# Kernel tuning notes

Measured on AMD Instinct MI355X. Metric: run time of the kernel, lower is better.

Reference implementation:

```python
import jax, jax.numpy as jnp
import numpy as np

SFREQ = 100
NPERSEG = 100  # min(n_times=200, 100)
NOVERLAP = NPERSEG // 2

# periodic hann window (scipy get_window('hann', N) with sym=False)
_WIN_NP = 0.5 - 0.5 * np.cos(2.0 * np.pi * np.arange(NPERSEG) / NPERSEG)
_WIN_SQ_SUM = float(np.sum(_WIN_NP ** 2))
_FREQS = np.fft.rfftfreq(NPERSEG, 1.0 / SFREQ)  # 0..50 Hz, 51 bins
_BANDS = [(0.5, 4.0), (4.0, 8.0), (8.0, 13.0), (13.0, 30.0)]  # delta/theta/alpha/beta
_BAND_IDX = [np.where((_FREQS >= lo) & (_FREQS <= hi))[0] for lo, hi in _BANDS]


def welch_band_features(x):
    """Batched Welch PSD band powers. x: (B,C,T) -> (B, C*4)."""
    B, C, T = x.shape
    step = NPERSEG - NOVERLAP
    n_seg = (T - NPERSEG) // step + 1
    seg_idx = np.arange(n_seg)[:, None] * step + np.arange(NPERSEG)  # (S, L)
    segs = x[..., seg_idx]                              # (B,C,S,L)
    segs = segs - segs.mean(-1, keepdims=True)          # detrend='constant'
    win = jnp.asarray(_WIN_NP, x.dtype)
    spec = jnp.fft.rfft(segs * win, axis=-1)            # (B,C,S,F)
    scale = 1.0 / (SFREQ * _WIN_SQ_SUM)
    psd = (spec.real ** 2 + spec.imag ** 2) * scale
    psd = psd.at[..., 1:-1].multiply(2.0)               # one-sided, nfft even
    psd = psd.mean(-2)                                  # average over segments -> (B,C,F)
    feats = jnp.stack([psd[..., idx].mean(-1) for idx in _BAND_IDX], axis=-1)  # (B,C,4)
    return feats.reshape(B, C * 4)


def setup_inputs() -> dict:
    key = jax.random.key(0)
    ks = jax.random.split(key, 16)
    B, C, T = 2048, 129, 200
    red = C // 8  # 16
    s = 0.05
    inp = {
        "x": jax.random.normal(ks[0], (B, C, T), jnp.float32),
        # channel attention fc (no bias)
        "w_att1": jax.random.normal(ks[1], (C, red), jnp.float32) * s,
        "w_att2": jax.random.normal(ks[2], (red, C), jnp.float32) * s,
        # stand-in EEGNeX backbone: time-mean pool + linear C->64
        "w_bb": jax.random.normal(ks[3], (C, 64), jnp.float32) * s,
        "b_bb": jnp.zeros((64,), jnp.float32),
        # freq encoder
        "w_fe1": jax.random.normal(ks[4], (C * 4, 128), jnp.float32) * s,
        "b_fe1": jnp.zeros((128,), jnp.float32),
        "w_fe2": jax.random.normal(ks[5], (128, 64), jnp.float32) * s,
        "b_fe2": jnp.zeros((64,), jnp.float32),
        # head
        "w_h1": jax.random.normal(ks[6], (128, 128), jnp.float32) * s,
        "b_h1": jnp.zeros((128,), jnp.float32),
        "w_h2": jax.random.normal(ks[7], (128, 64), jnp.float32) * s,
        "b_h2": jnp.zeros((64,), jnp.float32),
        "w_h3": jax.random.normal(ks[8], (64, 1), jnp.float32) * s,
        "b_h3": jnp.zeros((1,), jnp.float32),
    }
    return inp


def reference(x, w_att1, w_att2, w_bb, b_bb, w_fe1, b_fe1, w_fe2, b_fe2,
              w_h1, b_h1, w_h2, b_h2, w_h3, b_h3):
    # --- channel attention ---
    avg = x.mean(-1)                                    # (B,C)
    mx = x.max(-1)                                      # (B,C)
    fc = lambda v: jax.nn.relu(v @ w_att1) @ w_att2
    att = jax.nn.sigmoid(fc(avg) + fc(mx))[..., None]   # (B,C,1)
    x_att = x * att
    # --- backbone (stand-in for EEGNeXBase): time pool + linear ---
    time_feat = jax.nn.relu(x_att.mean(-1) @ w_bb + b_bb)  # (B,64)
    # --- frequency branch (computed from raw x, detached in original) ---
    freq = welch_band_features(jax.lax.stop_gradient(x))   # (B, C*4)
    freq = jax.nn.relu(freq @ w_fe1 + b_fe1)
    freq = jax.nn.relu(freq @ w_fe2 + b_fe2)               # (B,64)
    # --- head ---
    h = jnp.concatenate([time_feat, freq], axis=1)         # (B,128)
    h = jax.nn.relu(h @ w_h1 + b_h1)
    h = jax.nn.relu(h @ w_h2 + b_h2)
    return h @ w_h3 + b_h3                                  # (B,1)
```

## Files before the change

kernel.cpp:

```cpp
#include <hip/hip_runtime.h>
#include <math.h>

constexpr int BB = 2048;
constexpr int CC = 129;
constexpr int TT = 200;
constexpr int NPAIR = BB * CC;
constexpr int PPB = 64;
constexpr int XSTR = 201;

constexpr int OFF_AVG = 8192;
constexpr int OFF_MX  = OFF_AVG + NPAIR;
constexpr int OFF_FT  = OFF_MX + NPAIR;

__global__ void kInit(float2* __restrict__ tab) {
    int i = blockIdx.x * 256 + threadIdx.x;
    if (i >= 3000) return;
    int r = i / 100, t = i % 100;
    int ph = ((r + 1) * t) % 100;
    const float C = 0.06283185307179587f;
    float w = 0.5f - 0.5f * cosf(C * (float)t);
    float ang = C * (float)ph;
    tab[i] = make_float2(w * cosf(ang), w * sinf(ang));
}

template<int KB, int NB, bool STATS>
__device__ __forceinline__ void do_wave(const float* __restrict__ xp,
                                        const float* __restrict__ tbf,
                                        float* __restrict__ bs,
                                        int pair,
                                        float* __restrict__ avg,
                                        float* __restrict__ mxg) {
    const float* trow = tbf + (KB - 1) * 200;
    float re[NB][3], im[NB][3];
    #pragma unroll
    for (int b = 0; b < NB; b++)
        #pragma unroll
        for (int s = 0; s < 3; s++) { re[b][s] = 0.f; im[b][s] = 0.f; }
    float h0 = 0.f, h1 = 0.f, h2 = 0.f, h3 = 0.f, m = -3.4e38f;

    auto run = [&](int t0, int t1, float& hA, float& hC) {
        for (int t = t0; t < t1; t += 2) {
            float a0 = xp[t],       a1 = xp[t + 1];
            float b0 = xp[t + 50],  b1 = xp[t + 51];
            float c0 = xp[t + 100], c1 = xp[t + 101];
            if (STATS) {
                hA += a0 + a1; hC += c0 + c1;
                m = fmaxf(m, fmaxf(fmaxf(a0, a1), fmaxf(c0, c1)));
            }
            #pragma unroll
            for (int b = 0; b < NB; b++) {
                float4 w = *(const float4*)(trow + b * 200 + 2 * t);
                re[b][0] += a0 * w.x; im[b][0] += a0 * w.y;
                re[b][0] += a1 * w.z; im[b][0] += a1 * w.w;
                re[b][1] += b0 * w.x; im[b][1] += b0 * w.y;
                re[b][1] += b1 * w.z; im[b][1] += b1 * w.w;
                re[b][2] += c0 * w.x; im[b][2] += c0 * w.y;
                re[b][2] += c1 * w.z; im[b][2] += c1 * w.w;
            }
        }
    };
    run(0, 50, h0, h2);
    run(50, 100, h1, h3);

    if (STATS) {
        float mu0 = (h0 + h1) * 0.01f, mu1 = (h1 + h2) * 0.01f, mu2 = (h2 + h3) * 0.01f;
        re[0][0] += 25.f * mu0;
        re[0][1] += 25.f * mu1;
        re[0][2] += 25.f * mu2;
        avg[pair] = (h0 + h1 + h2 + h3) * (1.f / 200.f);
        mxg[pair] = m;
    }

    float s0 = 0.f, s1 = 0.f, s2 = 0.f, s3 = 0.f;
    #pragma unroll
    for (int b = 0; b < NB; b++) {
        int k = KB + b;
        float v = re[b][0] * re[b][0] + im[b][0] * im[b][0]
                + re[b][1] * re[b][1] + im[b][1] * im[b][1]
                + re[b][2] * re[b][2] + im[b][2] * im[b][2];
        if (k >= 1  && k <= 4)  s0 += v;
        if (k >= 4  && k <= 8)  s1 += v;
        if (k >= 8  && k <= 13) s2 += v;
        if (k >= 13 && k <= 30) s3 += v;
    }
    if (KB <= 4)                       atomicAdd(&bs[0], s0);
    if (KB <= 8 && KB + NB - 1 >= 4)   atomicAdd(&bs[1], s1);
    if (KB <= 13 && KB + NB - 1 >= 8)  atomicAdd(&bs[2], s2);
    if (KB + NB - 1 >= 13)             atomicAdd(&bs[3], s3);
}

__global__ __launch_bounds__(256, 2) void kA(const float* __restrict__ x,
                                             const float2* __restrict__ tabg,
                                             float* __restrict__ avg,
                                             float* __restrict__ mxg,
                                             float* __restrict__ feat) {
    __shared__ __align__(16) float xs[PPB * XSTR];
    __shared__ __align__(16) float tbf[6000];
    __shared__ float bsum[PPB][4];

    const int tid = threadIdx.x;
    const int blk = blockIdx.x;

    {
        const float4* tg = (const float4*)tabg;
        float4* td = (float4*)tbf;
        for (int i = tid; i < 1500; i += 256) td[i] = tg[i];
    }
    {
        const float4* xg = (const float4*)(x + (size_t)blk * PPB * TT);
        for (int i = tid; i < 3200; i += 256) {
            float4 v = xg[i];
            int p = i / 50, t4 = (i % 50) * 4;
            float* d = &xs[p * XSTR + t4];
            d[0] = v.x; d[1] = v.y; d[2] = v.z; d[3] = v.w;
        }
    }
    ((float*)bsum)[tid] = 0.f;
    __syncthreads();

    const int wv = tid >> 6, p = tid & 63;
    const float* xp = &xs[p * XSTR];
    float* bs = &bsum[p][0];
    const int pair = blk * PPB + p;

    if      (wv == 0) do_wave<1,  6, true >(xp, tbf, bs, pair, avg, mxg);
    else if (wv == 1) do_wave<7,  8, false>(xp, tbf, bs, pair, avg, mxg);
    else if (wv == 2) do_wave<15, 8, false>(xp, tbf, bs, pair, avg, mxg);
    else              do_wave<23, 8, false>(xp, tbf, bs, pair, avg, mxg);

    __syncthreads();
    {
        int pp = tid >> 2, bb = tid & 3;
        const float cnt[4] = {4.f, 5.f, 6.f, 18.f};
        feat[(size_t)(blk * PPB + pp) * 4 + bb] = bsum[pp][bb] * (2.f / (11250.f * cnt[bb]));
    }
}

__global__ __launch_bounds__(256) void kB(const float* __restrict__ avg,
                                          const float* __restrict__ mxv,
                                          const float* __restrict__ feat,
                                          const float* __restrict__ w_att1,
                                          const float* __restrict__ w_att2,
                                          const float* __restrict__ w_bb,
                                          const float* __restrict__ b_bb,
                                          const float* __restrict__ w_fe1,
                                          const float* __restrict__ b_fe1,
                                          const float* __restrict__ w_fe2,
                                          const float* __restrict__ b_fe2,
                                          const float* __restrict__ w_h1,
                                          const float* __restrict__ b_h1,
                                          const float* __restrict__ w_h2,
                                          const float* __restrict__ b_h2,
                                          const float* __restrict__ w_h3,
                                          const float* __restrict__ b_h3,
                                          float* __restrict__ out) {
    __shared__ __align__(16) float s_avg[258], s_mx[258], s_fq[1032];
    __shared__ float s_t1[32];
    __shared__ __align__(16) float s_v[258], s_h[256], s_f1[256], s_g1[256], s_g2[128];

    const int b = blockIdx.x;
    const int tid = threadIdx.x;

    for (int i = tid; i < 258; i += 256) { s_avg[i] = avg[b * 258 + i]; s_mx[i] = mxv[b * 258 + i]; }
    for (int i = tid; i < 1032; i += 256) s_fq[i] = feat[(size_t)b * 1032 + i];
    __syncthreads();

    if (tid < 32) {
        int r = tid >> 4, h = tid & 15;
        const float* pa = &s_avg[r * 129];
        const float* pm = &s_mx[r * 129];
        float a = 0.f, m = 0.f;
        for (int c = 0; c < 129; c++) {
            float w = w_att1[c * 16 + h];
            a += pa[c] * w; m += pm[c] * w;
        }
        s_t1[r * 16 + h] = fmaxf(a, 0.f) + fmaxf(m, 0.f);
    }
    __syncthreads();

    for (int i = tid; i < 258; i += 256) {
        int r = i / 129, c = i - r * 129;
        const float* t1 = &s_t1[r * 16];
        float l = 0.f;
        #pragma unroll
        for (int j = 0; j < 16; j++) l += t1[j] * w_att2[j * 129 + c];
        s_v[i] = s_avg[i] / (1.f + expf(-l));
    }
    __syncthreads();

    if (tid < 128) {
        int r = tid >> 6, o = tid & 63;
        const float* v = &s_v[r * 129];
        float acc = b_bb[o];
        for (int c = 0; c < 129; c++) acc += v[c] * w_bb[c * 64 + o];
        s_h[r * 128 + o] = fmaxf(acc, 0.f);
    }
    {
        int r = tid >> 7, o = tid & 127;
        const float* fq = &s_fq[r * 516];
        float acc = b_fe1[o];
        for (int i = 0; i < 516; i += 4) {
            float4 q = *(const float4*)(fq + i);
            acc += q.x * w_fe1[(i    ) * 128 + o];
            acc += q.y * w_fe1[(i + 1) * 128 + o];
            acc += q.z * w_fe1[(i + 2) * 128 + o];
            acc += q.w * w_fe1[(i + 3) * 128 + o];
        }
        s_f1[r * 128 + o] = fmaxf(acc, 0.f);
    }
    __syncthreads();

    if (tid < 128) {
        int r = tid >> 6, o = tid & 63;
        const float* f = &s_f1[r * 128];
        float acc = b_fe2[o];
        for (int i = 0; i < 128; i += 4) {
            float4 q = *(const float4*)(f + i);
            acc += q.x * w_fe2[(i    ) * 64 + o];
            acc += q.y * w_fe2[(i + 1) * 64 + o];
            acc += q.z * w_fe2[(i + 2) * 64 + o];
            acc += q.w * w_fe2[(i + 3) * 64 + o];
        }
        s_h[r * 128 + 64 + o] = fmaxf(acc, 0.f);
    }
    __syncthreads();

    {
        int r = tid >> 7, o = tid & 127;
        const float* hh = &s_h[r * 128];
        float acc = b_h1[o];
        for (int i = 0; i < 128; i += 4) {
            float4 q = *(const float4*)(hh + i);
            acc += q.x * w_h1[(i    ) * 128 + o];
            acc += q.y * w_h1[(i + 1) * 128 + o];
            acc += q.z * w_h1[(i + 2) * 128 + o];
            acc += q.w * w_h1[(i + 3) * 128 + o];
        }
        s_g1[r * 128 + o] = fmaxf(acc, 0.f);
    }
    __syncthreads();

    if (tid < 128) {
        int r = tid >> 6, o = tid & 63;
        const float* g = &s_g1[r * 128];
        float acc = b_h2[o];
        for (int i = 0; i < 128; i += 4) {
            float4 q = *(const float4*)(g + i);
            acc += q.x * w_h2[(i    ) * 64 + o];
            acc += q.y * w_h2[(i + 1) * 64 + o];
            acc += q.z * w_h2[(i + 2) * 64 + o];
            acc += q.w * w_h2[(i + 3) * 64 + o];
        }
        s_g2[r * 64 + o] = fmaxf(acc, 0.f);
    }
    __syncthreads();

    if (tid < 128) {
        int r = tid >> 6, o = tid & 63;
        float pz = s_g2[r * 64 + o] * w_h3[o];
        for (int off = 32; off >= 1; off >>= 1) pz += __shfl_xor(pz, off, 64);
        if (o == 0) out[b * 2 + r] = pz + b_h3[0];
    }
}

extern "C" void kernel_launch(void* const* d_in, const int* in_sizes, int n_in,
                              void* d_out, int out_size, void* d_ws, size_t ws_size,
                              hipStream_t stream) {
    const float* x      = (const float*)d_in[0];
    const float* w_att1 = (const float*)d_in[1];
    const float* w_att2 = (const float*)d_in[2];
    const float* w_bb   = (const float*)d_in[3];
    const float* b_bb   = (const float*)d_in[4];
    const float* w_fe1  = (const float*)d_in[5];
    const float* b_fe1  = (const float*)d_in[6];
    const float* w_fe2  = (const float*)d_in[7];
    const float* b_fe2  = (const float*)d_in[8];
    const float* w_h1   = (const float*)d_in[9];
    const float* b_h1   = (const float*)d_in[10];
    const float* w_h2   = (const float*)d_in[11];
    const float* b_h2   = (const float*)d_in[12];
    const float* w_h3   = (const float*)d_in[13];
    const float* b_h3   = (const float*)d_in[14];

    float* ws = (float*)d_ws;
    float2* tab = (float2*)ws;
    float* avg = ws + OFF_AVG;
    float* mxv = ws + OFF_MX;
    float* feat = ws + OFF_FT;

    kInit<<<12, 256, 0, stream>>>(tab);
    kA<<<NPAIR / PPB, 256, 0, stream>>>(x, (const float2*)tab, avg, mxv, feat);
    kB<<<BB / 2, 256, 0, stream>>>(avg, mxv, feat,
                                   w_att1, w_att2, w_bb, b_bb,
                                   w_fe1, b_fe1, w_fe2, b_fe2,
                                   w_h1, b_h1, w_h2, b_h2, w_h3, b_h3,
                                   (float*)d_out);
}
```

Baseline: 494.0 us.

## Split DFT bins across 8 waves, vectorize LDS reads, and split-K the MLP kernel

The Welch kernel now runs 512 threads per block, so eight waves each cover four frequency bins instead of four waves covering six to eight. The mean/max statistics move into a separate vectorized pass on wave 0. The x tile stride is padded to 204 so rows are 16-byte aligned, which allows float4 stores and loads in LDS, and the DFT inner loop is unrolled four samples at a time. The MLP kernel now handles one batch row per block, with split-K partial sums across all 256 threads for each layer. This adds more syncs and a redundant extra pass over x in LDS for the statistics, and the larger block may reduce per-thread register budget.

```diff
diff --git a/kernel.cpp b/kernel.cpp
--- a/kernel.cpp
+++ b/kernel.cpp
@@ -6,7 +6,7 @@
 constexpr int TT = 200;
 constexpr int NPAIR = BB * CC;
 constexpr int PPB = 64;
-constexpr int XSTR = 201;
+constexpr int XSTR = 204;
 
 constexpr int OFF_AVG = 8192;
 constexpr int OFF_MX  = OFF_AVG + NPAIR;
@@ -23,52 +23,46 @@
     tab[i] = make_float2(w * cosf(ang), w * sinf(ang));
 }
 
-template<int KB, int NB, bool STATS>
-__device__ __forceinline__ void do_wave(const float* __restrict__ xp,
-                                        const float* __restrict__ tbf,
-                                        float* __restrict__ bs,
-                                        int pair,
-                                        float* __restrict__ avg,
-                                        float* __restrict__ mxg) {
+template<int KB, int NB>
+__device__ __forceinline__ void dft_wave(const float* __restrict__ xp,
+                                         const float* __restrict__ tbf,
+                                         float* __restrict__ bs,
+                                         float mu0, float mu1, float mu2) {
     const float* trow = tbf + (KB - 1) * 200;
     float re[NB][3], im[NB][3];
     #pragma unroll
     for (int b = 0; b < NB; b++)
         #pragma unroll
         for (int s = 0; s < 3; s++) { re[b][s] = 0.f; im[b][s] = 0.f; }
-    float h0 = 0.f, h1 = 0.f, h2 = 0.f, h3 = 0.f, m = -3.4e38f;
-
-    auto run = [&](int t0, int t1, float& hA, float& hC) {
-        for (int t = t0; t < t1; t += 2) {
-            float a0 = xp[t],       a1 = xp[t + 1];
-            float b0 = xp[t + 50],  b1 = xp[t + 51];
-            float c0 = xp[t + 100], c1 = xp[t + 101];
-            if (STATS) {
-                hA += a0 + a1; hC += c0 + c1;
-                m = fmaxf(m, fmaxf(fmaxf(a0, a1), fmaxf(c0, c1)));
+
+    #pragma unroll 5
+    for (int t0 = 0; t0 < 100; t0 += 4) {
+        float4 a  = *(const float4*)(xp + t0);
+        float2 b0 = *(const float2*)(xp + t0 + 50);
+        float2 b1 = *(const float2*)(xp + t0 + 52);
+        float4 c  = *(const float4*)(xp + t0 + 100);
+        float xa[4] = {a.x, a.y, a.z, a.w};
+        float xb[4] = {b0.x, b0.y, b1.x, b1.y};
+        float xc[4] = {c.x, c.y, c.z, c.w};
+        #pragma unroll
+        for (int b = 0; b < NB; b++) {
+            float4 w0 = *(const float4*)(trow + b * 200 + 2 * t0);
+            float4 w1 = *(const float4*)(trow + b * 200 + 2 * t0 + 4);
+            float cs[4] = {w0.x, w0.z, w1.x, w1.z};
+            float sn[4] = {w0.y, w0.w, w1.y, w1.w};
+            #pragma unroll
+            for (int u = 0; u < 4; u++) {
+                re[b][0] += xa[u] * cs[u];  im[b][0] += xa[u] * sn[u];
+                re[b][1] += xb[u] * cs[u];  im[b][1] += xb[u] * sn[u];
+                re[b][2] += xc[u] * cs[u];  im[b][2] += xc[u] * sn[u];
             }
-            #pragma unroll
-            for (int b = 0; b < NB; b++) {
-                float4 w = *(const float4*)(trow + b * 200 + 2 * t);
-                re[b][0] += a0 * w.x; im[b][0] += a0 * w.y;
-                re[b][0] += a1 * w.z; im[b][0] += a1 * w.w;
-                re[b][1] += b0 * w.x; im[b][1] += b0 * w.y;
-                re[b][1] += b1 * w.z; im[b][1] += b1 * w.w;
-                re[b][2] += c0 * w.x; im[b][2] += c0 * w.y;
-                re[b][2] += c1 * w.z; im[b][2] += c1 * w.w;
-            }
-        }
-    };
-    run(0, 50, h0, h2);
-    run(50, 100, h1, h3);
-
-    if (STATS) {
-        float mu0 = (h0 + h1) * 0.01f, mu1 = (h1 + h2) * 0.01f, mu2 = (h2 + h3) * 0.01f;
+        }
+    }
+
+    if (KB == 1) {
         re[0][0] += 25.f * mu0;
         re[0][1] += 25.f * mu1;
         re[0][2] += 25.f * mu2;
-        avg[pair] = (h0 + h1 + h2 + h3) * (1.f / 200.f);
-        mxg[pair] = m;
     }
 
     float s0 = 0.f, s1 = 0.f, s2 = 0.f, s3 = 0.f;
@@ -81,7 +75,7 @@
         if (k >= 1  && k <= 4)  s0 += v;
         if (k >= 4  && k <= 8)  s1 += v;
         if (k >= 8  && k <= 13) s2 += v;
-        if (k >= 13 && k <= 30) s3 += v;
+        if (k >= 13)            s3 += v;
     }
     if (KB <= 4)                       atomicAdd(&bs[0], s0);
     if (KB <= 8 && KB + NB - 1 >= 4)   atomicAdd(&bs[1], s1);
@@ -89,7 +83,7 @@
     if (KB + NB - 1 >= 13)             atomicAdd(&bs[3], s3);
 }
 
-__global__ __launch_bounds__(256, 2) void kA(const float* __restrict__ x,
+__global__ __launch_bounds__(512, 4) void kA(const float* __restrict__ x,
                                              const float2* __restrict__ tabg,
                                              float* __restrict__ avg,
                                              float* __restrict__ mxg,
@@ -104,162 +98,194 @@
     {
         const float4* tg = (const float4*)tabg;
         float4* td = (float4*)tbf;
-        for (int i = tid; i < 1500; i += 256) td[i] = tg[i];
+        for (int i = tid; i < 1500; i += 512) td[i] = tg[i];
     }
     {
         const float4* xg = (const float4*)(x + (size_t)blk * PPB * TT);
-        for (int i = tid; i < 3200; i += 256) {
+        for (int i = tid; i < 3200; i += 512) {
             float4 v = xg[i];
             int p = i / 50, t4 = (i % 50) * 4;
-            float* d = &xs[p * XSTR + t4];
-            d[0] = v.x; d[1] = v.y; d[2] = v.z; d[3] = v.w;
-        }
-    }
-    ((float*)bsum)[tid] = 0.f;
+            *(float4*)(xs + p * XSTR + t4) = v;
+        }
+    }
+    if (tid < 256) ((float*)bsum)[tid] = 0.f;
     __syncthreads();
 
     const int wv = tid >> 6, p = tid & 63;
-    const float* xp = &xs[p * XSTR];
-    float* bs = &bsum[p][0];
-    const int pair = blk * PPB + p;
-
-    if      (wv == 0) do_wave<1,  6, true >(xp, tbf, bs, pair, avg, mxg);
-    else if (wv == 1) do_wave<7,  8, false>(xp, tbf, bs, pair, avg, mxg);
-    else if (wv == 2) do_wave<15, 8, false>(xp, tbf, bs, pair, avg, mxg);
-    else              do_wave<23, 8, false>(xp, tbf, bs, pair, avg, mxg);
-
-    __syncthreads();
-    {
+    const float* xp = xs + p * XSTR;
+    float* bs = bsum[p];
+
+    float mu0 = 0.f, mu1 = 0.f, mu2 = 0.f;
+    if (wv == 0) {
+        float h0 = 0.f, h1 = 0.f, h2 = 0.f, h3 = 0.f, m = -3.4e38f;
+        #pragma unroll
+        for (int i = 0; i < 12; i++) {
+            float4 v = *(const float4*)(xp + i * 4);
+            h0 += (v.x + v.y) + (v.z + v.w);
+            m = fmaxf(m, fmaxf(fmaxf(v.x, v.y), fmaxf(v.z, v.w)));
+        }
+        {   float4 v = *(const float4*)(xp + 48);
+            h0 += v.x + v.y; h1 += v.z + v.w;
+            m = fmaxf(m, fmaxf(fmaxf(v.x, v.y), fmaxf(v.z, v.w))); }
+        #pragma unroll
+        for (int i = 13; i < 25; i++) {
+            float4 v = *(const float4*)(xp + i * 4);
+            h1 += (v.x + v.y) + (v.z + v.w);
+            m = fmaxf(m, fmaxf(fmaxf(v.x, v.y), fmaxf(v.z, v.w)));
+        }
+        #pragma unroll
+        for (int i = 25; i < 37; i++) {
+            float4 v = *(const float4*)(xp + i * 4);
+            h2 += (v.x + v.y) + (v.z + v.w);
+            m = fmaxf(m, fmaxf(fmaxf(v.x, v.y), fmaxf(v.z, v.w)));
+        }
+        {   float4 v = *(const float4*)(xp + 148);
+            h2 += v.x + v.y; h3 += v.z + v.w;
+            m = fmaxf(m, fmaxf(fmaxf(v.x, v.y), fmaxf(v.z, v.w))); }
+        #pragma unroll
+        for (int i = 38; i < 50; i++) {
+            float4 v = *(const float4*)(xp + i * 4);
+            h3 += (v.x + v.y) + (v.z + v.w);
+            m = fmaxf(m, fmaxf(fmaxf(v.x, v.y), fmaxf(v.z, v.w)));
+        }
+        int pair = blk * PPB + p;
+        avg[pair] = (h0 + h1 + h2 + h3) * (1.f / 200.f);
+        mxg[pair] = m;
+        mu0 = (h0 + h1) * 0.01f; mu1 = (h1 + h2) * 0.01f; mu2 = (h2 + h3) * 0.01f;
+    }
+
+    switch (wv) {
+        case 0: dft_wave<1,  2>(xp, tbf, bs, mu0, mu1, mu2); break;
+        case 1: dft_wave<3,  4>(xp, tbf, bs, 0, 0, 0); break;
+        case 2: dft_wave<7,  4>(xp, tbf, bs, 0, 0, 0); break;
+        case 3: dft_wave<11, 4>(xp, tbf, bs, 0, 0, 0); break;
+        case 4: dft_wave<15, 4>(xp, tbf, bs, 0, 0, 0); break;
+        case 5: dft_wave<19, 4>(xp, tbf, bs, 0, 0, 0); break;
+        case 6: dft_wave<23, 4>(xp, tbf, bs, 0, 0, 0); break;
+        default: dft_wave<27, 4>(xp, tbf, bs, 0, 0, 0); break;
+    }
+
+    __syncthreads();
+    if (tid < 256) {
         int pp = tid >> 2, bb = tid & 3;
         const float cnt[4] = {4.f, 5.f, 6.f, 18.f};
         feat[(size_t)(blk * PPB + pp) * 4 + bb] = bsum[pp][bb] * (2.f / (11250.f * cnt[bb]));
     }
 }
 
-__global__ __launch_bounds__(256) void kB(const float* __restrict__ avg,
-                                          const float* __restrict__ mxv,
-                                          const float* __restrict__ feat,
-                                          const float* __restrict__ w_att1,
-                                          const float* __restrict__ w_att2,
-                                          const float* __restrict__ w_bb,
-                                          const float* __restrict__ b_bb,
-                                          const float* __restrict__ w_fe1,
-                                          const float* __restrict__ b_fe1,
-                                          const float* __restrict__ w_fe2,
-                                          const float* __restrict__ b_fe2,
-                                          const float* __restrict__ w_h1,
-                                          const float* __restrict__ b_h1,
-                                          const float* __restrict__ w_h2,
-                                          const float* __restrict__ b_h2,
-                                          const float* __restrict__ w_h3,
-                                          const float* __restrict__ b_h3,
-                                          float* __restrict__ out) {
-    __shared__ __align__(16) float s_avg[258], s_mx[258], s_fq[1032];
-    __shared__ float s_t1[32];
-    __shared__ __align__(16) float s_v[258], s_h[256], s_f1[256], s_g1[256], s_g2[128];
+__global__ __launch_bounds__(256, 8) void kB(const float* __restrict__ avg,
+                                             const float* __restrict__ mxv,
+                                             const float* __restrict__ feat,
+                                             const float* __restrict__ w_att1,
+                                             const float* __restrict__ w_att2,
+                                             const float* __restrict__ w_bb,
+                                             const float* __restrict__ b_bb,
+                                             const float* __restrict__ w_fe1,
+                                             const float* __restrict__ b_fe1,
+                                             const float* __restrict__ w_fe2,
+                                             const float* __restrict__ b_fe2,
+                                             const float* __restrict__ w_h1,
+                                             const float* __restrict__ b_h1,
+                                             const float* __restrict__ w_h2,
+                                             const float* __restrict__ b_h2,
+                                             const float* __restrict__ w_h3,
+                                             const float* __restrict__ b_h3,
+                                             float* __restrict__ out) {
+    __shared__ float s_avg[132], s_mx[132], s_fq[520];
+    __shared__ float s_t1a[16], s_t1b[16], s_t1[16];
+    __shared__ float s_v[132];
+    __shared__ float s_tf[2][64];
+    __shared__ float s_p1[2][128];
+    __shared__ float s_f1[128];
+    __shared__ float s_p2[4][64];
+    __shared__ float s_h[128];
+    __shared__ float s_pg1[2][128];
+    __shared__ float s_g1[128];
+    __shared__ float s_pg2[4][64];
 
     const int b = blockIdx.x;
     const int tid = threadIdx.x;
 
-    for (int i = tid; i < 258; i += 256) { s_avg[i] = avg[b * 258 + i]; s_mx[i] = mxv[b * 258 + i]; }
-    for (int i = tid; i < 1032; i += 256) s_fq[i] = feat[(size_t)b * 1032 + i];
+    for (int i = tid; i < 129; i += 256) { s_avg[i] = avg[b * 129 + i]; s_mx[i] = mxv[b * 129 + i]; }
+    for (int i = tid; i < 516; i += 256) s_fq[i] = feat[(size_t)b * 516 + i];
     __syncthreads();
 
     if (tid < 32) {
-        int r = tid >> 4, h = tid & 15;
-        const float* pa = &s_avg[r * 129];
-        const float* pm = &s_mx[r * 129];
-        float a = 0.f, m = 0.f;
-        for (int c = 0; c < 129; c++) {
-            float w = w_att1[c * 16 + h];
-            a += pa[c] * w; m += pm[c] * w;
-        }
-        s_t1[r * 16 + h] = fmaxf(a, 0.f) + fmaxf(m, 0.f);
-    }
-    __syncthreads();
-
-    for (int i = tid; i < 258; i += 256) {
-        int r = i / 129, c = i - r * 129;
-        const float* t1 = &s_t1[r * 16];
+        int h = tid & 15;
+        const float* src = (tid >= 16) ? s_mx : s_avg;
+        float acc = 0.f;
+        #pragma unroll 4
+        for (int c = 0; c < 129; c++) acc += src[c] * w_att1[c * 16 + h];
+        ((tid >= 16) ? s_t1b : s_t1a)[h] = fmaxf(acc, 0.f);
+    }
+    __syncthreads();
+    if (tid < 16) s_t1[tid] = s_t1a[tid] + s_t1b[tid];
+    __syncthreads();
+
+    if (tid < 129) {
         float l = 0.f;
         #pragma unroll
-        for (int j = 0; j < 16; j++) l += t1[j] * w_att2[j * 129 + c];
-        s_v[i] = s_avg[i] / (1.f + expf(-l));
+        for (int j = 0; j < 16; j++) l += s_t1[j] * w_att2[j * 129 + tid];
+        s_v[tid] = s_avg[tid] / (1.f + expf(-l));
     }
     __syncthreads();
 
     if (tid < 128) {
-        int r = tid >> 6, o = tid & 63;
-        const float* v = &s_v[r * 129];
-        float acc = b_bb[o];
-        for (int c = 0; c < 129; c++) acc += v[c] * w_bb[c * 64 + o];
-        s_h[r * 128 + o] = fmaxf(acc, 0.f);
-    }
-    {
-        int r = tid >> 7, o = tid & 127;
-        const float* fq = &s_fq[r * 516];
-        float acc = b_fe1[o];
-        for (int i = 0; i < 516; i += 4) {
-            float4 q = *(const float4*)(fq + i);
-            acc += q.x * w_fe1[(i    ) * 128 + o];
-            acc += q.y * w_fe1[(i + 1) * 128 + o];
-            acc += q.z * w_fe1[(i + 2) * 128 + o];
-            acc += q.w * w_fe1[(i + 3) * 128 + o];
-        }
-        s_f1[r * 128 + o] = fmaxf(acc, 0.f);
-    }
-    __syncthreads();
-
-    if (tid < 128) {
-        int r = tid >> 6, o = tid & 63;
-        const float* f = &s_f1[r * 128];
-        float acc = b_fe2[o];
-        for (int i = 0; i < 128; i += 4) {
-            float4 q = *(const float4*)(f + i);
-            acc += q.x * w_fe2[(i    ) * 64 + o];
-            acc += q.y * w_fe2[(i + 1) * 64 + o];
-            acc += q.z * w_fe2[(i + 2) * 64 + o];
-            acc += q.w * w_fe2[(i + 3) * 64 + o];
-        }
-        s_h[r * 128 + 64 + o] = fmaxf(acc, 0.f);
-    }
-    __syncthreads();
-
-    {
-        int r = tid >> 7, o = tid & 127;
-        const float* hh = &s_h[r * 128];
-        float acc = b_h1[o];
-        for (int i = 0; i < 128; i += 4) {
-            float4 q = *(const float4*)(hh + i);
-            acc += q.x * w_h1[(i    ) * 128 + o];
-            acc += q.y * w_h1[(i + 1) * 128 + o];
-            acc += q.z * w_h1[(i + 2) * 128 + o];
-            acc += q.w * w_h1[(i + 3) * 128 + o];
-        }
-        s_g1[r * 128 + o] = fmaxf(acc, 0.f);
-    }
-    __syncthreads();
-
-    if (tid < 128) {
-        int r = tid >> 6, o = tid & 63;
-        const float* g = &s_g1[r * 128];
-        float acc = b_h2[o];
-        for (int i = 0; i < 128; i += 4) {
-            float4 q = *(const float4*)(g + i);
-            acc += q.x * w_h2[(i    ) * 64 + o];
-            acc += q.y * w_h2[(i + 1) * 64 + o];
-            acc += q.z * w_h2[(i + 2) * 64 + o];
-            acc += q.w * w_h2[(i + 3) * 64 + o];
-        }
-        s_g2[r * 64 + o] = fmaxf(acc, 0.f);
-    }
-    __syncthreads();
-
-    if (tid < 128) {
-        int r = tid >> 6, o = tid & 63;
-        float pz = s_g2[r * 64 + o] * w_h3[o];
+        int o = tid & 63, ks = tid >> 6;
+        int i0 = ks ? 65 : 0, i1 = ks ? 129 : 65;
+        float acc = 0.f;
+        #pragma unroll 4
+        for (int i = i0; i < i1; i++) acc += s_v[i] * w_bb[i * 64 + o];
+        s_tf[ks][o] = acc;
+    }
+    {
+        int o = tid & 127, ks = tid >> 7;
+        float acc = 0.f;
+        #pragma unroll 4
+        for (int i = ks * 258; i < ks * 258 + 258; i++) acc += s_fq[i] * w_fe1[i * 128 + o];
+        s_p1[ks][o] = acc;
+    }
+    __syncthreads();
+    if (tid < 64) s_h[tid] = fmaxf(s_tf[0][tid] + s_tf[1][tid] + b_bb[tid], 0.f);
+    if (tid >= 128) { int o = tid - 128; s_f1[o] = fmaxf(s_p1[0][o] + s_p1[1][o] + b_fe1[o], 0.f); }
+    __syncthreads();
+
+    {
+        int o = tid & 63, ks = tid >> 6;
+        float acc = 0.f;
+        #pragma unroll 4
+        for (int i = ks * 32; i < ks * 32 + 32; i++) acc += s_f1[i] * w_fe2[i * 64 + o];
+        s_p2[ks][o] = acc;
+    }
+    __syncthreads();
+    if (tid < 64) s_h[64 + tid] = fmaxf(s_p2[0][tid] + s_p2[1][tid] + s_p2[2][tid] + s_p2[3][tid] + b_fe2[tid], 0.f);
+    __syncthreads();
+
+    {
+        int o = tid & 127, ks = tid >> 7;
+        float acc = 0.f;
+        #pragma unroll 4
+        for (int i = ks * 64; i < ks * 64 + 64; i++) acc += s_h[i] * w_h1[i * 128 + o];
+        s_pg1[ks][o] = acc;
+    }
+    __syncthreads();
+    if (tid < 128) s_g1[tid] = fmaxf(s_pg1[0][tid] + s_pg1[1][tid] + b_h1[tid], 0.f);
+    __syncthreads();
+
+    {
+        int o = tid & 63, ks = tid >> 6;
+        float acc = 0.f;
+        #pragma unroll 4
+        for (int i = ks * 32; i < ks * 32 + 32; i++) acc += s_g1[i] * w_h2[i * 64 + o];
+        s_pg2[ks][o] = acc;
+    }
+    __syncthreads();
+
+    if (tid < 64) {
+        float g2 = fmaxf(s_pg2[0][tid] + s_pg2[1][tid] + s_pg2[2][tid] + s_pg2[3][tid] + b_h2[tid], 0.f);
+        float pz = g2 * w_h3[tid];
         for (int off = 32; off >= 1; off >>= 1) pz += __shfl_xor(pz, off, 64);
-        if (o == 0) out[b * 2 + r] = pz + b_h3[0];
+        if (tid == 0) out[b] = pz + b_h3[0];
     }
 }
 
@@ -289,10 +315,10 @@
     float* feat = ws + OFF_FT;
 
     kInit<<<12, 256, 0, stream>>>(tab);
-    kA<<<NPAIR / PPB, 256, 0, stream>>>(x, (const float2*)tab, avg, mxv, feat);
-    kB<<<BB / 2, 256, 0, stream>>>(avg, mxv, feat,
-                                   w_att1, w_att2, w_bb, b_bb,
-                                   w_fe1, b_fe1, w_fe2, b_fe2,
-                                   w_h1, b_h1, w_h2, b_h2, w_h3, b_h3,
-                                   (float*)d_out);
-}
+    kA<<<NPAIR / PPB, 512, 0, stream>>>(x, (const float2*)tab, avg, mxv, feat);
+    kB<<<BB, 256, 0, stream>>>(avg, mxv, feat,
+                               w_att1, w_att2, w_bb, b_bb,
+                               w_fe1, b_fe1, w_fe2, b_fe2,
+                               w_h1, b_h1, w_h2, b_h2, w_h3, b_h3,
+                               (float*)d_out);
+}
```

New measurement: 570.0 us. +15.4%, slower.
